# Kernel optimization log

Measured on AMD Instinct MI355X. Metric: run time of the kernel, lower is better.

Reference implementation:

```python
import jax, jax.numpy as jnp
import numpy as np

HEADS = 8
DIM_HEAD = 64
DIM = 512
INNER = HEADS * DIM_HEAD  # 512
SCALE = DIM_HEAD ** -0.5


def setup_inputs() -> dict:
    key = jax.random.key(0)
    k1, k2, k3, k4 = jax.random.split(key, 4)
    b, n = 8, 4096
    x = jax.random.normal(k1, (b, n, DIM), dtype=jnp.float32)
    # torch Linear weight layout: [out_features, in_features]
    w_qkv = jax.random.normal(k2, (INNER * 3, DIM), dtype=jnp.float32) * (DIM ** -0.5)
    w_out = jax.random.normal(k3, (DIM, INNER), dtype=jnp.float32) * (INNER ** -0.5)
    b_out = jax.random.normal(k4, (DIM,), dtype=jnp.float32) * 0.01
    return {"x": x, "w_qkv": w_qkv, "w_out": w_out, "b_out": b_out}


def _feature_map(t):
    return jax.nn.elu(t) + 1.0


def reference(x, w_qkv, w_out, b_out):
    b, n, _ = x.shape
    h, d = HEADS, DIM_HEAD
    qkv = x @ w_qkv.T  # (b, n, 3*inner)
    q, k, v = jnp.split(qkv, 3, axis=-1)
    # (b, n, h*d) -> (b, h, n, d)
    reshape = lambda t: t.reshape(b, n, h, d).transpose(0, 2, 1, 3)
    q, k, v = reshape(q), reshape(k), reshape(v)
    q = _feature_map(q * SCALE)
    k = _feature_map(k)
    k_cumsum = k.sum(axis=2)  # (b, h, d)
    context = jnp.einsum('bhnd,bhne->bhde', k, v)
    out = jnp.einsum('bhnd,bhde->bhne', q, context)
    denom = jnp.einsum('bhnd,bhd->bhn', q, k_cumsum)[..., None] + 1e-8
    out = out / denom
    out = out.transpose(0, 2, 1, 3).reshape(b, n, h * d)
    return out @ w_out.T + b_out
```

## Files before the change

### kernel.cpp

```cpp
#include <hip/hip_runtime.h>
#include <cstdint>
#include <cstddef>

typedef __bf16 bf16_t;
typedef bf16_t bf16x8 __attribute__((ext_vector_type(8)));
typedef float f32x4 __attribute__((ext_vector_type(4)));
typedef unsigned short u16x8 __attribute__((ext_vector_type(8)));
typedef unsigned short u16x4 __attribute__((ext_vector_type(4)));

#define SEQ 4096
#define BATCH 8
#define NTOK 32768
#define NQKV 1536
#define DMODEL 512
#define NBH 64
#define NCHUNK 8
#define KSTEPS 8

__device__ __forceinline__ unsigned short f2b(float f) {
    union { float f; unsigned u; } c; c.f = f;
    unsigned u = c.u;
    u += 0x7fffu + ((u >> 16) & 1u);
    return (unsigned short)(u >> 16);
}
__device__ __forceinline__ float b2f(unsigned short h) {
    union { unsigned u; float f; } c; c.u = ((unsigned)h) << 16;
    return c.f;
}
__device__ __forceinline__ float feat(float v) {
    return v > 0.f ? v + 1.f : __expf(v);
}

__device__ __forceinline__ void gload16(const unsigned short* g, unsigned short* lds_base) {
    __builtin_amdgcn_global_load_lds((const __attribute__((address_space(1))) unsigned int*)g,
                                     (__attribute__((address_space(3))) unsigned int*)lds_base,
                                     16, 0, 0);
}

__device__ __forceinline__ void packW(const float* __restrict__ src,
                                      unsigned short* __restrict__ dst,
                                      int totalP4, int t0, int stride) {
    for (int j4 = t0; j4 < totalP4; j4 += stride) {
        int p = j4 << 2;
        int ke   = p & 7;
        int lane = (p >> 3) & 63;
        int ni   = (p >> 9) & 3;
        int kk   = (p >> 11) & 1;
        int wn   = (p >> 12) & 1;
        int kt   = (p >> 13) & 7;
        int bcol = p >> 16;
        int n = bcol * 128 + wn * 64 + ni * 16 + (lane & 15);
        int k = kt * 64 + kk * 32 + (lane >> 4) * 8 + ke;
        f32x4 v = *(const f32x4*)&src[(size_t)n * 512 + k];
        u16x4 o = { f2b(v[0]), f2b(v[1]), f2b(v[2]), f2b(v[3]) };
        ((u16x4*)dst)[j4] = o;
    }
}

__global__ __launch_bounds__(256) void prep_kernel(const float* __restrict__ x,
                                                   const float* __restrict__ wqkv,
                                                   const float* __restrict__ wout,
                                                   unsigned short* __restrict__ xB,
                                                   unsigned short* __restrict__ wqkvP,
                                                   unsigned short* __restrict__ woutP) {
    const int stride = gridDim.x * 256;
    const int t0 = blockIdx.x * 256 + threadIdx.x;
    for (int j = t0; j < NTOK * DMODEL / 4; j += stride) {
        f32x4 v = ((const f32x4*)x)[j];
        u16x4 o = { f2b(v[0]), f2b(v[1]), f2b(v[2]), f2b(v[3]) };
        ((u16x4*)xB)[j] = o;
    }
    packW(wqkv, wqkvP, NQKV * DMODEL / 4, t0, stride);
    packW(wout, woutP, DMODEL * DMODEL / 4, t0, stride);
}

template <int MODE>
__global__ __launch_bounds__(512, 4) void gemm_kernel(const unsigned short* __restrict__ A,
                                                      const unsigned short* __restrict__ Bp,
                                                      void* __restrict__ Cq,
                                                      unsigned short* __restrict__ Ck,
                                                      unsigned short* __restrict__ Cv,
                                                      const float* __restrict__ bias,
                                                      int M, int N, int K, int nColBlocks) {
    __shared__ __align__(16) unsigned short As_[2][256 * 64];
    const int tid = threadIdx.x;
    const int nwg = gridDim.x;
    int bid = blockIdx.x;
    if ((nwg & 7) == 0) bid = (bid & 7) * (nwg >> 3) + (bid >> 3);
    const int brow = bid / nColBlocks, bcol = bid % nColBlocks;
    const int rowBase = brow * 256, colBase = bcol * 128;
    const int lane = tid & 63, wv = tid >> 6;
    const int wm = wv >> 1, wn = wv & 1;
    const int lr = lane & 15, lk = lane >> 4;
    const int xorv = (lr & 7) << 4;
    const int sr8 = (wv << 3) + (lane >> 3);
    const int ss = lane & 7;

    f32x4 acc[4][4] = {};

    const unsigned short* bwl = Bp + ((size_t)bcol << 16) + ((size_t)wn << 12) + (lane << 3);

    auto stageA = [&](int buf, int kt) {
        #pragma unroll
        for (int j = 0; j < 4; ++j) {
            int r = j * 64 + sr8;
            int scol = ((ss ^ (r & 7)) << 3) + kt;
            gload16(A + (size_t)(rowBase + r) * K + scol, &As_[buf][(j * 512 + (wv << 6)) * 8]);
        }
    };

    stageA(0, 0);

    #pragma unroll
    for (int t = 0; t < KSTEPS; ++t) {
        __syncthreads();
        bf16x8 bfr[2][4];
        #pragma unroll
        for (int kk = 0; kk < 2; ++kk)
            #pragma unroll
            for (int ni = 0; ni < 4; ++ni)
                bfr[kk][ni] = *(const bf16x8*)(bwl + (t << 13) + (kk << 11) + (ni << 9));
        __builtin_amdgcn_sched_barrier(0);
        if (t + 1 < KSTEPS) stageA((t + 1) & 1, (t + 1) << 6);

        const unsigned short* Ab = &As_[t & 1][0];
        #pragma unroll
        for (int kk = 0; kk < 2; ++kk) {
            bf16x8 af[4];
            #pragma unroll
            for (int mi = 0; mi < 4; ++mi) {
                int row = wm * 64 + mi * 16 + lr;
                af[mi] = *(const bf16x8*)((const char*)Ab + row * 128 + ((kk * 64 + lk * 16) ^ xorv));
            }
            #pragma unroll
            for (int mi = 0; mi < 4; ++mi)
                #pragma unroll
                for (int ni = 0; ni < 4; ++ni)
                    acc[mi][ni] = __builtin_amdgcn_mfma_f32_16x16x32_bf16(af[mi], bfr[kk][ni], acc[mi][ni], 0, 0, 0);
        }
    }

    if (MODE == 1) {
        #pragma unroll
        for (int mi = 0; mi < 4; ++mi) {
            const int grow0 = rowBase + wm * 64 + mi * 16 + lk * 4;
            #pragma unroll
            for (int ni = 0; ni < 4; ++ni) {
                const int gcol = colBase + wn * 64 + ni * 16 + lr;
                #pragma unroll
                for (int r = 0; r < 4; ++r)
                    ((float*)Cq)[(size_t)(grow0 + r) * DMODEL + gcol] = acc[mi][ni][r] + bias[gcol];
            }
        }
    } else if (colBase < 512) {
        #pragma unroll
        for (int mi = 0; mi < 4; ++mi) {
            const int grow0 = rowBase + wm * 64 + mi * 16 + lk * 4;
            #pragma unroll
            for (int ni = 0; ni < 4; ++ni) {
                const int gcol = colBase + wn * 64 + ni * 16 + lr;
                #pragma unroll
                for (int r = 0; r < 4; ++r)
                    ((unsigned short*)Cq)[(size_t)(grow0 + r) * DMODEL + gcol] =
                        f2b(feat(acc[mi][ni][r] * 0.125f));
            }
        }
    } else if (colBase < 1024) {
        #pragma unroll
        for (int mi = 0; mi < 4; ++mi) {
            const int grow0 = rowBase + wm * 64 + mi * 16 + lk * 4;
            const int b_ = grow0 >> 12, n0 = grow0 & 4095;
            #pragma unroll
            for (int ni = 0; ni < 4; ++ni) {
                const int hd = colBase - 512 + wn * 64 + ni * 16 + lr;
                u16x4 o = { f2b(feat(acc[mi][ni][0])), f2b(feat(acc[mi][ni][1])),
                            f2b(feat(acc[mi][ni][2])), f2b(feat(acc[mi][ni][3])) };
                *(u16x4*)&Ck[((size_t)(b_ * 512 + hd)) * SEQ + n0] = o;
            }
        }
    } else {
        #pragma unroll
        for (int mi = 0; mi < 4; ++mi) {
            const int grow0 = rowBase + wm * 64 + mi * 16 + lk * 4;
            const int b_ = grow0 >> 12, n0 = grow0 & 4095;
            #pragma unroll
            for (int ni = 0; ni < 4; ++ni) {
                const int hd = colBase - 1024 + wn * 64 + ni * 16 + lr;
                u16x4 o = { f2b(acc[mi][ni][0]), f2b(acc[mi][ni][1]),
                            f2b(acc[mi][ni][2]), f2b(acc[mi][ni][3]) };
                *(u16x4*)&Cv[((size_t)(b_ * 512 + hd)) * SEQ + n0] = o;
            }
        }
    }
}

__global__ __launch_bounds__(256) void ctx_kernel(const unsigned short* __restrict__ kT,
                                                  const unsigned short* __restrict__ vT,
                                                  float* __restrict__ ctxP,
                                                  float* __restrict__ kcP) {
    const int bh = blockIdx.x >> 3;
    const int chunk = blockIdx.x & 7;
    __shared__ __align__(16) unsigned short ks[64 * 64];
    __shared__ __align__(16) unsigned short vs[64 * 64];
    const int tid = threadIdx.x;
    const int lane = tid & 63, wv = tid >> 6;
    const int lr = lane & 15, lk = lane >> 4;
    const int xorv = (lr & 7) << 4;
    const int r_s = tid >> 3, s_s = tid & 7;
    const unsigned short* kg = kT + (size_t)bh * 64 * SEQ;
    const unsigned short* vg = vT + (size_t)bh * 64 * SEQ;

    f32x4 acc[4] = {};
    f32x4 kacc[4] = {};
    union { u16x8 u; bf16x8 b; } onesc;
    onesc.u = (u16x8){0x3F80, 0x3F80, 0x3F80, 0x3F80, 0x3F80, 0x3F80, 0x3F80, 0x3F80};
    const bf16x8 ones = onesc.b;

    for (int t = 0; t < 8; ++t) {
        const int n0 = chunk * 512 + t * 64;
        __syncthreads();
        #pragma unroll
        for (int j = 0; j < 2; ++j) {
            int r = j * 32 + r_s;
            int scol = ((s_s ^ (r & 7)) << 3) + n0;
            gload16(kg + (size_t)r * SEQ + scol, ks + (j * 256 + (wv << 6)) * 8);
            gload16(vg + (size_t)r * SEQ + scol, vs + (j * 256 + (wv << 6)) * 8);
        }
        __syncthreads();
        #pragma unroll
        for (int kk = 0; kk < 2; ++kk) {
            bf16x8 bfr = *(const bf16x8*)((const char*)vs + (wv * 16 + lr) * 128 + ((kk * 64 + lk * 16) ^ xorv));
            #pragma unroll
            for (int mi = 0; mi < 4; ++mi) {
                bf16x8 af = *(const bf16x8*)((const char*)ks + (mi * 16 + lr) * 128 + ((kk * 64 + lk * 16) ^ xorv));
                acc[mi] = __builtin_amdgcn_mfma_f32_16x16x32_bf16(af, bfr, acc[mi], 0, 0, 0);
                if (wv == 0)
                    kacc[mi] = __builtin_amdgcn_mfma_f32_16x16x32_bf16(af, ones, kacc[mi], 0, 0, 0);
            }
        }
    }
    float* cp = ctxP + ((size_t)chunk * NBH + bh) * 4096;
    #pragma unroll
    for (int mi = 0; mi < 4; ++mi)
        #pragma unroll
        for (int r = 0; r < 4; ++r)
            cp[(mi * 16 + lk * 4 + r) * 64 + wv * 16 + lr] = acc[mi][r];
    if (wv == 0 && lr == 0) {
        float* kp = kcP + ((size_t)chunk * NBH + bh) * 64;
        #pragma unroll
        for (int mi = 0; mi < 4; ++mi)
            #pragma unroll
            for (int r = 0; r < 4; ++r)
                kp[mi * 16 + lk * 4 + r] = kacc[mi][r];
    }
}

__global__ __launch_bounds__(256) void reduce_kernel(const float* __restrict__ ctxP,
                                                     const float* __restrict__ kcP,
                                                     unsigned short* __restrict__ cTh,
                                                     unsigned short* __restrict__ cTl,
                                                     float* __restrict__ kcR) {
    const int bh = blockIdx.x;
    const int t = threadIdx.x;
    #pragma unroll
    for (int p = 0; p < 4; ++p) {
        int idx = p * 256 + t;
        f32x4 s = {0.f, 0.f, 0.f, 0.f};
        for (int c = 0; c < NCHUNK; ++c)
            s += ((const f32x4*)(ctxP + ((size_t)c * NBH + bh) * 4096))[idx];
        int d = idx >> 4, e0 = (idx & 15) * 4;
        #pragma unroll
        for (int j = 0; j < 4; ++j) {
            unsigned short hi = f2b(s[j]);
            cTh[(size_t)bh * 4096 + (e0 + j) * 64 + d] = hi;
            cTl[(size_t)bh * 4096 + (e0 + j) * 64 + d] = f2b(s[j] - b2f(hi));
        }
    }
    if (t < 64) {
        float s = 0.f;
        for (int c = 0; c < NCHUNK; ++c) s += kcP[((size_t)c * NBH + bh) * 64 + t];
        kcR[bh * 64 + t] = s;
    }
}

__global__ __launch_bounds__(256) void attn_kernel(const unsigned short* __restrict__ qF,
                                                   const unsigned short* __restrict__ cTh,
                                                   const unsigned short* __restrict__ cTl,
                                                   const float* __restrict__ kcR,
                                                   unsigned short* __restrict__ inner) {
    const int bh = blockIdx.x >> 6;
    const int rt = blockIdx.x & 63;
    const int b = bh >> 3, h = bh & 7;
    const size_t rowBase = (size_t)b * SEQ + (size_t)rt * 64;
    __shared__ __align__(16) unsigned short qs[64 * 64];
    __shared__ __align__(16) unsigned short chs[64 * 64];
    __shared__ __align__(16) unsigned short cls[64 * 64];
    __shared__ float dpart[64][4];
    __shared__ float dens[64];
    __shared__ float kcs[64];
    const int tid = threadIdx.x;
    const int lane = tid & 63, wv = tid >> 6;
    const int lr = lane & 15, lk = lane >> 4;
    const int xorv = (lr & 7) << 4;
    const int r_s = tid >> 3, s_s = tid & 7;

    #pragma unroll
    for (int j = 0; j < 2; ++j) {
        int r = j * 32 + r_s;
        int sc = (s_s ^ (r & 7)) << 3;
        gload16(qF + (rowBase + r) * DMODEL + h * 64 + sc, qs + (j * 256 + (wv << 6)) * 8);
        gload16(cTh + (size_t)bh * 4096 + r * 64 + sc, chs + (j * 256 + (wv << 6)) * 8);
        gload16(cTl + (size_t)bh * 4096 + r * 64 + sc, cls + (j * 256 + (wv << 6)) * 8);
    }
    if (tid < 64) kcs[tid] = kcR[bh * 64 + tid];
    __syncthreads();
    {
        int row = tid & 63, part = tid >> 6;
        float s = 0.f;
        #pragma unroll
        for (int i = 0; i < 16; ++i) {
            int d = part * 16 + i;
            unsigned short qv = *(const unsigned short*)((const char*)qs + row * 128 + ((d * 2) ^ ((row & 7) << 4)));
            s += b2f(qv) * kcs[d];
        }
        dpart[row][part] = s;
    }
    __syncthreads();
    if (tid < 64) dens[tid] = 1e-8f + dpart[tid][0] + dpart[tid][1] + dpart[tid][2] + dpart[tid][3];
    __syncthreads();

    f32x4 acc[4] = {};
    #pragma unroll
    for (int kk = 0; kk < 2; ++kk) {
        bf16x8 af = *(const bf16x8*)((const char*)qs + (wv * 16 + lr) * 128 + ((kk * 64 + lk * 16) ^ xorv));
        #pragma unroll
        for (int ni = 0; ni < 4; ++ni) {
            bf16x8 bh_ = *(const bf16x8*)((const char*)chs + (ni * 16 + lr) * 128 + ((kk * 64 + lk * 16) ^ xorv));
            bf16x8 bl_ = *(const bf16x8*)((const char*)cls + (ni * 16 + lr) * 128 + ((kk * 64 + lk * 16) ^ xorv));
            acc[ni] = __builtin_amdgcn_mfma_f32_16x16x32_bf16(af, bh_, acc[ni], 0, 0, 0);
            acc[ni] = __builtin_amdgcn_mfma_f32_16x16x32_bf16(af, bl_, acc[ni], 0, 0, 0);
        }
    }
    #pragma unroll
    for (int ni = 0; ni < 4; ++ni)
        #pragma unroll
        for (int r = 0; r < 4; ++r) {
            int n = wv * 16 + lk * 4 + r;
            float o = acc[ni][r] / dens[n];
            inner[(rowBase + n) * DMODEL + h * 64 + ni * 16 + lr] = f2b(o);
        }
}

extern "C" void kernel_launch(void* const* d_in, const int* in_sizes, int n_in,
                              void* d_out, int out_size, void* d_ws, size_t ws_size,
                              hipStream_t stream) {
    (void)in_sizes; (void)n_in; (void)out_size; (void)ws_size;
    const float* x    = (const float*)d_in[0];
    const float* wqkv = (const float*)d_in[1];
    const float* wout = (const float*)d_in[2];
    const float* bout = (const float*)d_in[3];

    char* w = (char*)d_ws;
    unsigned short* xB    = (unsigned short*)(w);
    float*          ctxP  = (float*)(w);
    float*          kcP   = (float*)(w + 8388608);
    unsigned short* inner = (unsigned short*)(w);
    unsigned short* qF    = (unsigned short*)(w + 33554432);
    unsigned short* kT    = (unsigned short*)(w + 67108864);
    unsigned short* vT    = (unsigned short*)(w + 100663296);
    unsigned short* wqkvP = (unsigned short*)(w + 134217728);
    unsigned short* woutP = (unsigned short*)(w + 135790592);
    unsigned short* cTh   = (unsigned short*)(w + 136314880);
    unsigned short* cTl   = (unsigned short*)(w + 136839168);
    float*          kcR   = (float*)(w + 137363456);

    hipLaunchKernelGGL(prep_kernel, dim3(2048), dim3(256), 0, stream,
                       x, wqkv, wout, xB, wqkvP, woutP);
    hipLaunchKernelGGL((gemm_kernel<0>), dim3(1536), dim3(512), 0, stream,
                       xB, wqkvP, (void*)qF, kT, vT, (const float*)nullptr,
                       NTOK, NQKV, DMODEL, 12);
    hipLaunchKernelGGL(ctx_kernel, dim3(NBH * NCHUNK), dim3(256), 0, stream, kT, vT, ctxP, kcP);
    hipLaunchKernelGGL(reduce_kernel, dim3(NBH), dim3(256), 0, stream, ctxP, kcP, cTh, cTl, kcR);
    hipLaunchKernelGGL(attn_kernel, dim3(NBH * 64), dim3(256), 0, stream, qF, cTh, cTl, kcR, inner);
    hipLaunchKernelGGL((gemm_kernel<1>), dim3(512), dim3(512), 0, stream,
                       inner, woutP, (void*)d_out, (unsigned short*)nullptr, (unsigned short*)nullptr, bout,
                       NTOK, DMODEL, DMODEL, 4);
}
```

Before: 156.4 us.

## Keep full-K A row panel resident in LDS and loop over output column panels

The GEMM kernel now loads a 128-row by 512-K block of A into shared memory once. It then loops over all output column panels, reading B fragments straight from global memory, so A is not re-read for every column block. The grid shrinks to 256 workgroups with 128 KB of LDS each, and the double-buffered K pipeline is dropped. This trades A reuse for lower occupancy (one workgroup per CU), no overlap of loads with compute, and only 256 workgroups to spread over the CUs.

```diff
diff --git a/kernel.cpp b/kernel.cpp
--- a/kernel.cpp
+++ b/kernel.cpp
@@ -75,120 +75,112 @@
 }
 
 template <int MODE>
-__global__ __launch_bounds__(512, 4) void gemm_kernel(const unsigned short* __restrict__ A,
-                                                      const unsigned short* __restrict__ Bp,
-                                                      void* __restrict__ Cq,
-                                                      unsigned short* __restrict__ Ck,
-                                                      unsigned short* __restrict__ Cv,
-                                                      const float* __restrict__ bias,
-                                                      int M, int N, int K, int nColBlocks) {
-    __shared__ __align__(16) unsigned short As_[2][256 * 64];
+__global__ __launch_bounds__(512) void gemm_kernel(const unsigned short* __restrict__ A,
+                                                   const unsigned short* __restrict__ Bp,
+                                                   void* __restrict__ Cq,
+                                                   unsigned short* __restrict__ Ck,
+                                                   unsigned short* __restrict__ Cv,
+                                                   const float* __restrict__ bias,
+                                                   int K, int nPanels) {
+    __shared__ __align__(16) unsigned short As_[128 * 512];
     const int tid = threadIdx.x;
     const int nwg = gridDim.x;
     int bid = blockIdx.x;
     if ((nwg & 7) == 0) bid = (bid & 7) * (nwg >> 3) + (bid >> 3);
-    const int brow = bid / nColBlocks, bcol = bid % nColBlocks;
-    const int rowBase = brow * 256, colBase = bcol * 128;
+    const int rowBase = bid * 128;
     const int lane = tid & 63, wv = tid >> 6;
-    const int wm = wv >> 1, wn = wv & 1;
+    const int wm = wv >> 2, wc = wv & 3;
+    const int wn = wc >> 1;
+    const int nodd = wc & 1;
     const int lr = lane & 15, lk = lane >> 4;
-    const int xorv = (lr & 7) << 4;
-    const int sr8 = (wv << 3) + (lane >> 3);
-    const int ss = lane & 7;
-
-    f32x4 acc[4][4] = {};
-
-    const unsigned short* bwl = Bp + ((size_t)bcol << 16) + ((size_t)wn << 12) + (lane << 3);
-
-    auto stageA = [&](int buf, int kt) {
-        #pragma unroll
-        for (int j = 0; j < 4; ++j) {
-            int r = j * 64 + sr8;
-            int scol = ((ss ^ (r & 7)) << 3) + kt;
-            gload16(A + (size_t)(rowBase + r) * K + scol, &As_[buf][(j * 512 + (wv << 6)) * 8]);
-        }
-    };
-
-    stageA(0, 0);
-
-    #pragma unroll
-    for (int t = 0; t < KSTEPS; ++t) {
-        __syncthreads();
-        bf16x8 bfr[2][4];
-        #pragma unroll
-        for (int kk = 0; kk < 2; ++kk)
-            #pragma unroll
-            for (int ni = 0; ni < 4; ++ni)
-                bfr[kk][ni] = *(const bf16x8*)(bwl + (t << 13) + (kk << 11) + (ni << 9));
-        __builtin_amdgcn_sched_barrier(0);
-        if (t + 1 < KSTEPS) stageA((t + 1) & 1, (t + 1) << 6);
-
-        const unsigned short* Ab = &As_[t & 1][0];
-        #pragma unroll
-        for (int kk = 0; kk < 2; ++kk) {
-            bf16x8 af[4];
-            #pragma unroll
-            for (int mi = 0; mi < 4; ++mi) {
-                int row = wm * 64 + mi * 16 + lr;
-                af[mi] = *(const bf16x8*)((const char*)Ab + row * 128 + ((kk * 64 + lk * 16) ^ xorv));
-            }
-            #pragma unroll
-            for (int mi = 0; mi < 4; ++mi)
-                #pragma unroll
-                for (int ni = 0; ni < 4; ++ni)
-                    acc[mi][ni] = __builtin_amdgcn_mfma_f32_16x16x32_bf16(af[mi], bfr[kk][ni], acc[mi][ni], 0, 0, 0);
-        }
-    }
-
-    if (MODE == 1) {
-        #pragma unroll
-        for (int mi = 0; mi < 4; ++mi) {
-            const int grow0 = rowBase + wm * 64 + mi * 16 + lk * 4;
-            #pragma unroll
-            for (int ni = 0; ni < 4; ++ni) {
-                const int gcol = colBase + wn * 64 + ni * 16 + lr;
-                #pragma unroll
-                for (int r = 0; r < 4; ++r)
-                    ((float*)Cq)[(size_t)(grow0 + r) * DMODEL + gcol] = acc[mi][ni][r] + bias[gcol];
-            }
-        }
-    } else if (colBase < 512) {
-        #pragma unroll
-        for (int mi = 0; mi < 4; ++mi) {
-            const int grow0 = rowBase + wm * 64 + mi * 16 + lk * 4;
-            #pragma unroll
-            for (int ni = 0; ni < 4; ++ni) {
-                const int gcol = colBase + wn * 64 + ni * 16 + lr;
-                #pragma unroll
-                for (int r = 0; r < 4; ++r)
-                    ((unsigned short*)Cq)[(size_t)(grow0 + r) * DMODEL + gcol] =
-                        f2b(feat(acc[mi][ni][r] * 0.125f));
-            }
-        }
-    } else if (colBase < 1024) {
-        #pragma unroll
-        for (int mi = 0; mi < 4; ++mi) {
-            const int grow0 = rowBase + wm * 64 + mi * 16 + lk * 4;
-            const int b_ = grow0 >> 12, n0 = grow0 & 4095;
-            #pragma unroll
-            for (int ni = 0; ni < 4; ++ni) {
-                const int hd = colBase - 512 + wn * 64 + ni * 16 + lr;
-                u16x4 o = { f2b(feat(acc[mi][ni][0])), f2b(feat(acc[mi][ni][1])),
-                            f2b(feat(acc[mi][ni][2])), f2b(feat(acc[mi][ni][3])) };
-                *(u16x4*)&Ck[((size_t)(b_ * 512 + hd)) * SEQ + n0] = o;
-            }
-        }
-    } else {
-        #pragma unroll
-        for (int mi = 0; mi < 4; ++mi) {
-            const int grow0 = rowBase + wm * 64 + mi * 16 + lk * 4;
-            const int b_ = grow0 >> 12, n0 = grow0 & 4095;
-            #pragma unroll
-            for (int ni = 0; ni < 4; ++ni) {
-                const int hd = colBase - 1024 + wn * 64 + ni * 16 + lr;
-                u16x4 o = { f2b(acc[mi][ni][0]), f2b(acc[mi][ni][1]),
-                            f2b(acc[mi][ni][2]), f2b(acc[mi][ni][3]) };
-                *(u16x4*)&Cv[((size_t)(b_ * 512 + hd)) * SEQ + n0] = o;
+
+    #pragma unroll
+    for (int j = 0; j < 16; ++j) {
+        int row = j * 8 + wv;
+        int slot = (lane & 56) | ((lane & 7) ^ (row & 7));
+        gload16(A + (size_t)(rowBase + row) * K + slot * 8, As_ + row * 512 + lane * 8);
+    }
+    __syncthreads();
+
+    for (int panel = 0; panel < nPanels; ++panel) {
+        const unsigned short* bpp = Bp + ((size_t)panel << 16) + (wn << 12) + ((nodd * 2) << 9) + (lane << 3);
+        f32x4 acc[4][2] = {};
+        #pragma unroll
+        for (int kt = 0; kt < KSTEPS; ++kt) {
+            bf16x8 bfr[2][2];
+            #pragma unroll
+            for (int kk = 0; kk < 2; ++kk)
+                #pragma unroll
+                for (int nj = 0; nj < 2; ++nj)
+                    bfr[kk][nj] = *(const bf16x8*)(bpp + (kt << 13) + (kk << 11) + (nj << 9));
+            #pragma unroll
+            for (int kk = 0; kk < 2; ++kk) {
+                bf16x8 af[4];
+                #pragma unroll
+                for (int mi = 0; mi < 4; ++mi) {
+                    int row = wm * 64 + mi * 16 + lr;
+                    af[mi] = *(const bf16x8*)((const char*)As_ + row * 1024 +
+                                              ((kt * 128 + kk * 64 + lk * 16) ^ ((row & 7) << 4)));
+                }
+                #pragma unroll
+                for (int mi = 0; mi < 4; ++mi)
+                    #pragma unroll
+                    for (int nj = 0; nj < 2; ++nj)
+                        acc[mi][nj] = __builtin_amdgcn_mfma_f32_16x16x32_bf16(af[mi], bfr[kk][nj], acc[mi][nj], 0, 0, 0);
+            }
+        }
+
+        const int colBase = panel * 128;
+        if (MODE == 1) {
+            #pragma unroll
+            for (int mi = 0; mi < 4; ++mi) {
+                const int grow0 = rowBase + wm * 64 + mi * 16 + lk * 4;
+                #pragma unroll
+                for (int nj = 0; nj < 2; ++nj) {
+                    const int gcol = colBase + wn * 64 + (nodd * 2 + nj) * 16 + lr;
+                    #pragma unroll
+                    for (int r = 0; r < 4; ++r)
+                        ((float*)Cq)[(size_t)(grow0 + r) * DMODEL + gcol] = acc[mi][nj][r] + bias[gcol];
+                }
+            }
+        } else if (colBase < 512) {
+            #pragma unroll
+            for (int mi = 0; mi < 4; ++mi) {
+                const int grow0 = rowBase + wm * 64 + mi * 16 + lk * 4;
+                #pragma unroll
+                for (int nj = 0; nj < 2; ++nj) {
+                    const int gcol = colBase + wn * 64 + (nodd * 2 + nj) * 16 + lr;
+                    #pragma unroll
+                    for (int r = 0; r < 4; ++r)
+                        ((unsigned short*)Cq)[(size_t)(grow0 + r) * DMODEL + gcol] =
+                            f2b(feat(acc[mi][nj][r] * 0.125f));
+                }
+            }
+        } else if (colBase < 1024) {
+            #pragma unroll
+            for (int mi = 0; mi < 4; ++mi) {
+                const int grow0 = rowBase + wm * 64 + mi * 16 + lk * 4;
+                const int b_ = grow0 >> 12, n0 = grow0 & 4095;
+                #pragma unroll
+                for (int nj = 0; nj < 2; ++nj) {
+                    const int hd = colBase - 512 + wn * 64 + (nodd * 2 + nj) * 16 + lr;
+                    u16x4 o = { f2b(feat(acc[mi][nj][0])), f2b(feat(acc[mi][nj][1])),
+                                f2b(feat(acc[mi][nj][2])), f2b(feat(acc[mi][nj][3])) };
+                    *(u16x4*)&Ck[((size_t)(b_ * 512 + hd)) * SEQ + n0] = o;
+                }
+            }
+        } else {
+            #pragma unroll
+            for (int mi = 0; mi < 4; ++mi) {
+                const int grow0 = rowBase + wm * 64 + mi * 16 + lk * 4;
+                const int b_ = grow0 >> 12, n0 = grow0 & 4095;
+                #pragma unroll
+                for (int nj = 0; nj < 2; ++nj) {
+                    const int hd = colBase - 1024 + wn * 64 + (nodd * 2 + nj) * 16 + lr;
+                    u16x4 o = { f2b(acc[mi][nj][0]), f2b(acc[mi][nj][1]),
+                                f2b(acc[mi][nj][2]), f2b(acc[mi][nj][3]) };
+                    *(u16x4*)&Cv[((size_t)(b_ * 512 + hd)) * SEQ + n0] = o;
+                }
             }
         }
     }
@@ -376,13 +368,13 @@
 
     hipLaunchKernelGGL(prep_kernel, dim3(2048), dim3(256), 0, stream,
                        x, wqkv, wout, xB, wqkvP, woutP);
-    hipLaunchKernelGGL((gemm_kernel<0>), dim3(1536), dim3(512), 0, stream,
+    hipLaunchKernelGGL((gemm_kernel<0>), dim3(256), dim3(512), 0, stream,
                        xB, wqkvP, (void*)qF, kT, vT, (const float*)nullptr,
-                       NTOK, NQKV, DMODEL, 12);
+                       DMODEL, 12);
     hipLaunchKernelGGL(ctx_kernel, dim3(NBH * NCHUNK), dim3(256), 0, stream, kT, vT, ctxP, kcP);
     hipLaunchKernelGGL(reduce_kernel, dim3(NBH), dim3(256), 0, stream, ctxP, kcP, cTh, cTl, kcR);
     hipLaunchKernelGGL(attn_kernel, dim3(NBH * 64), dim3(256), 0, stream, qF, cTh, cTl, kcR, inner);
-    hipLaunchKernelGGL((gemm_kernel<1>), dim3(512), dim3(512), 0, stream,
+    hipLaunchKernelGGL((gemm_kernel<1>), dim3(256), dim3(512), 0, stream,
                        inner, woutP, (void*)d_out, (unsigned short*)nullptr, (unsigned short*)nullptr, bout,
-                       NTOK, DMODEL, DMODEL, 4);
-}
+                       DMODEL, 4);
+}
```

Result: slower. 320.8 us (+105.1%).
